# Performance work log

Measured on AMD Instinct MI355X. Metric: run time of the kernel, lower is better.

## Reference

```python
import jax, jax.numpy as jnp
import numpy as np
import math

B, N, D, H, CD = 2, 384, 256, 8, 3
HD = D // H

def _linear_init(key, out_f, in_f):
    k1, k2 = jax.random.split(key)
    bound = 1.0 / math.sqrt(in_f)
    w = jax.random.uniform(k1, (out_f, in_f), jnp.float32, -bound, bound)
    b = jax.random.uniform(k2, (out_f,), jnp.float32, -bound, bound)
    return w, b

def setup_inputs() -> dict:
    key = jax.random.key(0)
    ks = jax.random.split(key, 7)
    x = jax.random.normal(ks[0], (B, N, D), jnp.float32)
    coords = jax.random.normal(ks[1], (B, N, CD), jnp.float32)
    qkv_w, qkv_b = _linear_init(ks[2], 3 * D, D)
    rb_w1, rb_b1 = _linear_init(ks[3], D, CD)
    rb_w2, rb_b2 = _linear_init(ks[4], H, D)
    rv_w1, rv_b1 = _linear_init(ks[5], D, CD)
    rv_w2, rv_b2 = _linear_init(ks[6], D, D)
    return {"x": x, "coords": coords, "qkv_w": qkv_w, "qkv_b": qkv_b,
            "rb_w1": rb_w1, "rb_b1": rb_b1, "rb_w2": rb_w2, "rb_b2": rb_b2,
            "rv_w1": rv_w1, "rv_b1": rv_b1, "rv_w2": rv_w2, "rv_b2": rv_b2}

def reference(x, coords, qkv_w, qkv_b, rb_w1, rb_b1, rb_w2, rb_b2, rv_w1, rv_b1, rv_w2, rv_b2):
    # QKV projection -> (B, H, N, HD) each
    qkv = x @ qkv_w.T + qkv_b
    q, k, v = jnp.split(qkv, 3, axis=-1)
    to_heads = lambda t: t.reshape(B, N, H, HD).transpose(0, 2, 1, 3)
    qh, kh, vh = to_heads(q), to_heads(k), to_heads(v)

    # pairwise relative coordinates: (B, N, N, CD)
    rel = coords[:, :, None, :] - coords[:, None, :, :]

    # rel_bias MLP: (B, N, N, H) -> (B, H, N, N)
    rel_bias = jax.nn.silu(rel @ rb_w1.T + rb_b1) @ rb_w2.T + rb_b2
    rel_bias = rel_bias.transpose(0, 3, 1, 2)

    # rel_value MLP: (B, N, N, D) -> (B, H, N, N, HD)
    rel_value = jax.nn.silu(rel @ rv_w1.T + rv_b1) @ rv_w2.T + rv_b2
    rel_value = rel_value.reshape(B, N, N, H, HD).transpose(0, 3, 1, 2, 4)

    # attn_mask=None path: all-true boolean mask -> additive term is zero
    scores = jnp.einsum('bhid,bhjd->bhij', qh, kh) / math.sqrt(float(HD)) + rel_bias
    weights = jax.nn.softmax(scores, axis=-1)

    base = jnp.einsum('bhij,bhjd->bhid', weights, vh)
    rel_context = jnp.einsum('bhij,bhijd->bhid', weights, rel_value)
    context = base + rel_context  # (B, H, N, HD)
    return context.transpose(0, 2, 1, 3).reshape(B, N, D)
```

## Files before the change

### kernel.cpp

```cpp
#include <hip/hip_runtime.h>
#include <math.h>

#define BB 2
#define NN 384
#define DD 256
#define HH 8
#define RN (BB * NN)
#define INV_SQRT_HD 0.17677669529663687f
#define LOG2E 1.4426950408889634f
#define NLN2 -0.6931471805599453f
#define QSCALE (INV_SQRT_HD * LOG2E)

#define W2_ST 264
#define T_ST  264
#define EB_ST 392

typedef float f32x4 __attribute__((ext_vector_type(4)));
typedef __bf16 bf16x8 __attribute__((ext_vector_type(8)));
typedef __bf16 bf16x4 __attribute__((ext_vector_type(4)));

__device__ __forceinline__ f32x4 mfma16(bf16x8 a, bf16x8 b, f32x4 c) {
    return __builtin_amdgcn_mfma_f32_16x16x32_bf16(a, b, c, 0, 0, 0);
}

__device__ __forceinline__ float hidp(float d) {
    float e = __builtin_amdgcn_exp2f(d);
    return d * __builtin_amdgcn_rcpf(1.0f + e);
}
__device__ __forceinline__ bf16x8 hid8(bf16x8 av, float4 a0, float4 a1) {
    bf16x8 r;
    r[0] = (__bf16)hidp((float)av[0] - a0.x);
    r[1] = (__bf16)hidp((float)av[1] - a0.y);
    r[2] = (__bf16)hidp((float)av[2] - a0.z);
    r[3] = (__bf16)hidp((float)av[3] - a0.w);
    r[4] = (__bf16)hidp((float)av[4] - a1.x);
    r[5] = (__bf16)hidp((float)av[5] - a1.y);
    r[6] = (__bf16)hidp((float)av[6] - a1.z);
    r[7] = (__bf16)hidp((float)av[7] - a1.w);
    return r;
}
__device__ __forceinline__ bf16x8 hid8s(bf16x8 av, float a) {
    bf16x8 r;
#pragma unroll
    for (int q = 0; q < 8; ++q) r[q] = (__bf16)hidp((float)av[q] - a);
    return r;
}
__device__ __forceinline__ bf16x8 pack8(float4 a, float4 b) {
    bf16x8 r;
    r[0] = (__bf16)a.x; r[1] = (__bf16)a.y; r[2] = (__bf16)a.z; r[3] = (__bf16)a.w;
    r[4] = (__bf16)b.x; r[5] = (__bf16)b.y; r[6] = (__bf16)b.z; r[7] = (__bf16)b.w;
    return r;
}
__device__ __forceinline__ float selv(f32x4 v, int r) {
    return (r == 0) ? v[0] : (r == 1) ? v[1] : (r == 2) ? v[2] : v[3];
}

__global__ __launch_bounds__(256) void prep_kernel(
    const float* __restrict__ x, const float* __restrict__ coords,
    const float* __restrict__ qkv_w, const float* __restrict__ qkv_b,
    const float* __restrict__ rb_w1, const float* __restrict__ rv_w1,
    const float* __restrict__ rb_w2,
    float* __restrict__ qb, __bf16* __restrict__ kbbf, __bf16* __restrict__ vT,
    __bf16* __restrict__ Arb, __bf16* __restrict__ ArvT, __bf16* __restrict__ Arv,
    __bf16* __restrict__ w2neg)
{
    int bid = blockIdx.x, tid = threadIdx.x;
    if (bid >= 1344) {
        int idx = tid * 8;
        float4 wa = *(const float4*)(rb_w2 + idx);
        float4 wb = *(const float4*)(rb_w2 + idx + 4);
        float4 na = make_float4(-wa.x, -wa.y, -wa.z, -wa.w);
        float4 nb = make_float4(-wb.x, -wb.y, -wb.z, -wb.w);
        *(bf16x8*)(w2neg + idx) = pack8(na, nb);
        return;
    }
    if (bid >= 576) {
        int r = bid - 576, c = tid;
        float cx = coords[r * 3 + 0], cy = coords[r * 3 + 1], cz = coords[r * 3 + 2];
        float ab = (cx * rb_w1[c * 3] + cy * rb_w1[c * 3 + 1] + cz * rb_w1[c * 3 + 2]) * LOG2E;
        float av = (cx * rv_w1[c * 3] + cy * rv_w1[c * 3 + 1] + cz * rv_w1[c * 3 + 2]) * LOG2E;
        Arb[r * DD + c] = (__bf16)ab;
        ArvT[c * RN + r] = (__bf16)av;
        Arv[r * DD + c] = (__bf16)av;
        return;
    }
    int mt = bid % 48, nb = bid / 48;
    int w = tid >> 6, l = tid & 63, lr = l & 15, lg = l >> 4;
    int m0 = mt * 16, n0 = nb * 64 + w * 16;
    const float* xr = x + (size_t)(m0 + lr) * DD;
    const float* wr = qkv_w + (size_t)(n0 + lr) * DD;
    f32x4 acc = {0.f, 0.f, 0.f, 0.f};
#pragma unroll
    for (int ks = 0; ks < 8; ++ks) {
        int c0 = ks * 32 + lg * 8;
        float4 xa = *(const float4*)(xr + c0);
        float4 xb = *(const float4*)(xr + c0 + 4);
        float4 wa = *(const float4*)(wr + c0);
        float4 wb = *(const float4*)(wr + c0 + 4);
        acc = mfma16(pack8(xa, xb), pack8(wa, wb), acc);
    }
    int col = n0 + lr;
    float bo = qkv_b[col];
    int part = col >> 8, o = col & 255;
#pragma unroll
    for (int r = 0; r < 4; ++r) {
        int m = m0 + lg * 4 + r;
        float v = acc[r] + bo;
        if (part == 0) {
            qb[(size_t)m * DD + o] = v * QSCALE;
        } else if (part == 1) {
            kbbf[(size_t)m * DD + o] = (__bf16)v;
        } else {
            int b = (m >= NN) ? 1 : 0;
            int n = m - b * NN;
            vT[(size_t)b * DD * NN + (size_t)o * NN + n] = (__bf16)v;
        }
    }
}

__global__ __launch_bounds__(256, 4) void k2a_kernel(
    const float* __restrict__ rb_b1, const __bf16* __restrict__ w2neg,
    const float* __restrict__ rb_b2,
    const float* __restrict__ qb, const __bf16* __restrict__ kbbf,
    const __bf16* __restrict__ Arb,
    __bf16* __restrict__ eG, float* __restrict__ Zpart)
{
    __shared__ __align__(16) __bf16 qsbf[2][DD];
    __shared__ __align__(16) float Apr[2][DD];
    __shared__ __align__(16) __bf16 w2bf[HH * W2_ST];
    __shared__ float redsm[4][2][HH];

    int tid = threadIdx.x;
    int bid = blockIdx.x;
    int gp = bid >> 1, half = bid & 1;
    int gi0 = gp * 2;
    int b = (gp >= 192) ? 1 : 0;

    qsbf[0][tid] = (__bf16)qb[(size_t)gi0 * DD + tid];
    qsbf[1][tid] = (__bf16)qb[(size_t)(gi0 + 1) * DD + tid];
    float b1l = rb_b1[tid] * LOG2E;
    Apr[0][tid] = (float)Arb[(size_t)gi0 * DD + tid] + b1l;
    Apr[1][tid] = (float)Arb[(size_t)(gi0 + 1) * DD + tid] + b1l;
    {
        int idx = tid * 8;
        *(bf16x8*)&w2bf[(idx >> 8) * W2_ST + (idx & 255)] =
            *(const bf16x8*)(w2neg + idx);
    }
    __syncthreads();

    int l = tid & 63, wv = tid >> 6;
    int lr = l & 15, lg = l >> 4;
    float rb2l = rb_b2[lr & 7] * LOG2E;

    int jb0 = half * 192 + wv * 16;
    int jb1 = jb0 + 64, jb2 = jb0 + 128;
    const __bf16* arbB = Arb + (size_t)b * NN * DD;
    const __bf16* kbB  = kbbf + (size_t)b * NN * DD;
    const __bf16* ar0 = arbB + (size_t)(jb0 + lr) * DD;
    const __bf16* ar1 = arbB + (size_t)(jb1 + lr) * DD;
    const __bf16* ar2 = arbB + (size_t)(jb2 + lr) * DD;
    const __bf16* kr0 = kbB  + (size_t)(jb0 + lr) * DD;
    const __bf16* kr1 = kbB  + (size_t)(jb1 + lr) * DD;
    const __bf16* kr2 = kbB  + (size_t)(jb2 + lr) * DD;
    const __bf16* wfp = &w2bf[(lr & 7) * W2_ST];

    bf16x8 qf0_reg = *(const bf16x8*)&qsbf[0][(lr & 7) * 32 + lg * 8];
    bf16x8 qf1_reg = *(const bf16x8*)&qsbf[1][(lr & 7) * 32 + lg * 8];
    bf16x8 zero8;
#pragma unroll
    for (int e = 0; e < 8; ++e) zero8[e] = (__bf16)0.f;

    f32x4 zzz = {0.f, 0.f, 0.f, 0.f};
    f32x4 a00 = zzz, a01 = zzz, a02 = zzz;
    f32x4 a10 = zzz, a11 = zzz, a12 = zzz;
#pragma unroll
    for (int ks = 0; ks < 8; ++ks) {
        int c0 = ks * 32 + lg * 8;
        bf16x8 v0 = *(const bf16x8*)(ar0 + c0);
        bf16x8 v1 = *(const bf16x8*)(ar1 + c0);
        bf16x8 v2 = *(const bf16x8*)(ar2 + c0);
        bf16x8 k0 = *(const bf16x8*)(kr0 + c0);
        bf16x8 k1 = *(const bf16x8*)(kr1 + c0);
        bf16x8 k2 = *(const bf16x8*)(kr2 + c0);
        bf16x8 wf = *(const bf16x8*)(wfp + c0);
        float4 p00 = *(const float4*)&Apr[0][c0];
        float4 p01 = *(const float4*)&Apr[0][c0 + 4];
        float4 p10 = *(const float4*)&Apr[1][c0];
        float4 p11 = *(const float4*)&Apr[1][c0 + 4];
        bf16x8 q0 = (lr == ks) ? qf0_reg : zero8;
        bf16x8 q1 = (lr == ks) ? qf1_reg : zero8;
        a00 = mfma16(hid8(v0, p00, p01), wf, a00);
        a10 = mfma16(hid8(v0, p10, p11), wf, a10);
        a01 = mfma16(hid8(v1, p00, p01), wf, a01);
        a11 = mfma16(hid8(v1, p10, p11), wf, a11);
        a02 = mfma16(hid8(v2, p00, p01), wf, a02);
        a12 = mfma16(hid8(v2, p10, p11), wf, a12);
        a00 = mfma16(k0, q0, a00);
        a10 = mfma16(k0, q1, a10);
        a01 = mfma16(k1, q0, a01);
        a11 = mfma16(k1, q1, a11);
        a02 = mfma16(k2, q0, a02);
        a12 = mfma16(k2, q1, a12);
    }

    float z0 = 0.f, z1 = 0.f;
#define FINTILE(ACC, GI, JB, ZACC) { \
        float e0 = __builtin_amdgcn_exp2f(ACC[0] + rb2l); \
        float e1 = __builtin_amdgcn_exp2f(ACC[1] + rb2l); \
        float e2 = __builtin_amdgcn_exp2f(ACC[2] + rb2l); \
        float e3 = __builtin_amdgcn_exp2f(ACC[3] + rb2l); \
        if (lr < 8) { \
            bf16x4 ev; \
            ev[0] = (__bf16)e0; ev[1] = (__bf16)e1; \
            ev[2] = (__bf16)e2; ev[3] = (__bf16)e3; \
            *(bf16x4*)&eG[((size_t)(GI) * HH + lr) * NN + (JB) + lg * 4] = ev; \
        } \
        float zs = e0 + e1 + e2 + e3; \
        zs += __shfl_xor(zs, 16); \
        zs += __shfl_xor(zs, 32); \
        ZACC += zs; }
    FINTILE(a00, gi0,     jb0, z0)
    FINTILE(a01, gi0,     jb1, z0)
    FINTILE(a02, gi0,     jb2, z0)
    FINTILE(a10, gi0 + 1, jb0, z1)
    FINTILE(a11, gi0 + 1, jb1, z1)
    FINTILE(a12, gi0 + 1, jb2, z1)
#undef FINTILE
    if (lg == 0 && lr < 8) {
        redsm[wv][0][lr] = z0;
        redsm[wv][1][lr] = z1;
    }
    __syncthreads();
    if (tid < 16) {
        int g = tid >> 3, h = tid & 7;
        Zpart[((size_t)(gi0 + g) * 2 + half) * 8 + h] =
            redsm[0][g][h] + redsm[1][g][h] + redsm[2][g][h] + redsm[3][g][h];
    }
}

__global__ __launch_bounds__(256, 4) void k2b_kernel(
    const float* __restrict__ rv_b1, const float* __restrict__ rv_w2,
    const __bf16* __restrict__ vT, const __bf16* __restrict__ ArvT,
    const __bf16* __restrict__ Arv, const __bf16* __restrict__ eG,
    float* __restrict__ rcpart, float* __restrict__ basef)
{
    __shared__ __align__(16) float Apv[2][DD];
    __shared__ __align__(16) float Tl[2][HH * T_ST];
    __shared__ __align__(16) __bf16 els[16 * EB_ST];

    int tid = threadIdx.x;
    int bid = blockIdx.x;
    int gp = bid >> 1, ch = bid & 1;
    int gi0 = gp * 2;
    int b = (gp >= 192) ? 1 : 0;

    float b1l = rv_b1[tid] * LOG2E;
    Apv[0][tid] = (float)Arv[(size_t)gi0 * DD + tid] + b1l;
    Apv[1][tid] = (float)Arv[(size_t)(gi0 + 1) * DD + tid] + b1l;
    {
        int r = tid >> 4, cg = tid & 15;
        const __bf16* src = eG + (size_t)(gi0 * 8 + r) * NN;
#pragma unroll
        for (int s = 0; s < 3; ++s) {
            int col = s * 128 + cg * 8;
            *(bf16x8*)&els[r * EB_ST + col] = *(const bf16x8*)(src + col);
        }
    }
    __syncthreads();

    int l = tid & 63, wv = tid >> 6;
    int lr = l & 15, lg = l >> 4;

    int c0 = ch * 128 + wv * 16 + lr;
    int c1 = c0 + 64;
    float ap00 = Apv[0][c0], ap01 = Apv[0][c1];
    float ap10 = Apv[1][c0], ap11 = Apv[1][c1];
    const __bf16* vr0 = ArvT + (size_t)c0 * RN + b * NN;
    const __bf16* vr1 = ArvT + (size_t)c1 * RN + b * NN;
    const __bf16* tv0 = vT + (size_t)b * DD * NN + (size_t)c0 * NN;
    const __bf16* tv1 = vT + (size_t)b * DD * NN + (size_t)c1 * NN;

    f32x4 zzz = {0.f, 0.f, 0.f, 0.f};
    f32x4 T00 = zzz, T01 = zzz, T10 = zzz, T11 = zzz;
    f32x4 B0 = zzz, B1 = zzz;
#pragma unroll
    for (int ks = 0; ks < 12; ++ks) {
        int j0 = ks * 32 + lg * 8;
        bf16x8 ef  = *(const bf16x8*)&els[lr * EB_ST + j0];
        bf16x8 av0 = *(const bf16x8*)(vr0 + j0);
        bf16x8 av1 = *(const bf16x8*)(vr1 + j0);
        bf16x8 w0  = *(const bf16x8*)(tv0 + j0);
        bf16x8 w1  = *(const bf16x8*)(tv1 + j0);
        T00 = mfma16(ef, hid8s(av0, ap00), T00);
        T01 = mfma16(ef, hid8s(av1, ap01), T01);
        T10 = mfma16(ef, hid8s(av0, ap10), T10);
        T11 = mfma16(ef, hid8s(av1, ap11), T11);
        B0  = mfma16(ef, w0, B0);
        B1  = mfma16(ef, w1, B1);
    }

    if (lg < 2) {
#pragma unroll
        for (int r = 0; r < 4; ++r) {
            int h = lg * 4 + r;
            Tl[0][h * T_ST + c0] = T00[r] * NLN2;
            Tl[0][h * T_ST + c1] = T01[r] * NLN2;
        }
    } else {
#pragma unroll
        for (int r = 0; r < 4; ++r) {
            int h = (lg - 2) * 4 + r;
            Tl[1][h * T_ST + c0] = T10[r] * NLN2;
            Tl[1][h * T_ST + c1] = T11[r] * NLN2;
        }
    }
    {
        int h0 = c0 >> 5;
        if (lg == (h0 >> 2))     basef[(size_t)gi0 * DD + c0]       = selv(B0, h0 & 3);
        if (lg == 2 + (h0 >> 2)) basef[(size_t)(gi0 + 1) * DD + c0] = selv(B0, h0 & 3);
        int h1 = c1 >> 5;
        if (lg == (h1 >> 2))     basef[(size_t)gi0 * DD + c1]       = selv(B1, h1 & 3);
        if (lg == 2 + (h1 >> 2)) basef[(size_t)(gi0 + 1) * DD + c1] = selv(B1, h1 & 3);
    }
    __syncthreads();

    {
        int o = tid, h = o >> 5;
        const float4* w2p = (const float4*)(rv_w2 + (size_t)o * DD);
        const float* t0 = &Tl[0][h * T_ST];
        const float* t1 = &Tl[1][h * T_ST];
        float a0 = 0.f, a1 = 0.f;
#pragma unroll 4
        for (int cc = 0; cc < 32; ++cc) {
            int cidx = ch * 32 + cc;
            float4 wv4 = w2p[cidx];
            float4 u0 = *(const float4*)&t0[cidx * 4];
            float4 u1 = *(const float4*)&t1[cidx * 4];
            a0 += wv4.x * u0.x + wv4.y * u0.y + wv4.z * u0.z + wv4.w * u0.w;
            a1 += wv4.x * u1.x + wv4.y * u1.y + wv4.z * u1.z + wv4.w * u1.w;
        }
        rcpart[((size_t)ch * RN + gi0) * DD + o] = a0;
        rcpart[((size_t)ch * RN + gi0 + 1) * DD + o] = a1;
    }
}

__global__ __launch_bounds__(256) void k2c_kernel(
    const float* __restrict__ rcpart, const float* __restrict__ basef,
    const float* __restrict__ Zpart, const float* __restrict__ rv_b2,
    float* __restrict__ out)
{
    int gi = blockIdx.x, o = threadIdx.x, h = o >> 5;
    float z = Zpart[(size_t)gi * 16 + h] + Zpart[(size_t)gi * 16 + 8 + h];
    float rc = rcpart[(size_t)gi * DD + o] + rcpart[((size_t)RN + gi) * DD + o];
    out[(size_t)gi * DD + o] =
        (rc + basef[(size_t)gi * DD + o]) * __builtin_amdgcn_rcpf(z) + rv_b2[o];
}

extern "C" void kernel_launch(void* const* d_in, const int* in_sizes, int n_in,
                              void* d_out, int out_size, void* d_ws, size_t ws_size,
                              hipStream_t stream) {
    const float* x      = (const float*)d_in[0];
    const float* coords = (const float*)d_in[1];
    const float* qkv_w  = (const float*)d_in[2];
    const float* qkv_b  = (const float*)d_in[3];
    const float* rb_w1  = (const float*)d_in[4];
    const float* rb_b1  = (const float*)d_in[5];
    const float* rb_w2  = (const float*)d_in[6];
    const float* rb_b2  = (const float*)d_in[7];
    const float* rv_w1  = (const float*)d_in[8];
    const float* rv_b1  = (const float*)d_in[9];
    const float* rv_w2  = (const float*)d_in[10];
    const float* rv_b2  = (const float*)d_in[11];
    float* out = (float*)d_out;

    float* ws = (float*)d_ws;
    const int PER = RN * DD;
    float* qb = ws;
    __bf16* bfb  = (__bf16*)(ws + PER);
    __bf16* kbbf = bfb;
    __bf16* vTb  = bfb + PER;
    __bf16* Arb  = bfb + 2 * PER;
    __bf16* ArvT = bfb + 3 * PER;
    __bf16* Arv  = bfb + 4 * PER;
    __bf16* eG   = bfb + 5 * (size_t)PER;
    float* Zpart = (float*)(eG + (size_t)RN * HH * NN);
    float* basef = Zpart + (size_t)RN * 2 * HH;
    float* rcpart = basef + PER;
    __bf16* w2neg = (__bf16*)(rcpart + 2 * (size_t)PER);

    prep_kernel<<<1345, 256, 0, stream>>>(x, coords, qkv_w, qkv_b,
                                          rb_w1, rv_w1, rb_w2,
                                          qb, kbbf, vTb, Arb, ArvT, Arv, w2neg);
    k2a_kernel<<<RN, 256, 0, stream>>>(rb_b1, w2neg, rb_b2,
                                       qb, kbbf, Arb, eG, Zpart);
    k2b_kernel<<<RN, 256, 0, stream>>>(rv_b1, rv_w2,
                                       vTb, ArvT, Arv, eG, rcpart, basef);
    k2c_kernel<<<RN, 256, 0, stream>>>(rcpart, basef, Zpart, rv_b2, out);
}
```

Before: 75.81 us.

## Process four query rows per block in attention kernels to reuse key-side loads

```diff
diff --git a/kernel.cpp b/kernel.cpp
--- a/kernel.cpp
+++ b/kernel.cpp
@@ -12,8 +12,8 @@
 #define QSCALE (INV_SQRT_HD * LOG2E)
 
 #define W2_ST 264
-#define T_ST  264
 #define EB_ST 392
+#define TB_ST 264
 
 typedef float f32x4 __attribute__((ext_vector_type(4)));
 typedef __bf16 bf16x8 __attribute__((ext_vector_type(8)));
@@ -125,22 +125,23 @@
     const __bf16* __restrict__ Arb,
     __bf16* __restrict__ eG, float* __restrict__ Zpart)
 {
-    __shared__ __align__(16) __bf16 qsbf[2][DD];
-    __shared__ __align__(16) float Apr[2][DD];
+    __shared__ __align__(16) __bf16 qsbf[4][DD];
+    __shared__ __align__(16) float Apr[4][DD];
     __shared__ __align__(16) __bf16 w2bf[HH * W2_ST];
-    __shared__ float redsm[4][2][HH];
+    __shared__ float redsm[4][4][HH];
 
     int tid = threadIdx.x;
     int bid = blockIdx.x;
-    int gp = bid >> 1, half = bid & 1;
-    int gi0 = gp * 2;
-    int b = (gp >= 192) ? 1 : 0;
-
-    qsbf[0][tid] = (__bf16)qb[(size_t)gi0 * DD + tid];
-    qsbf[1][tid] = (__bf16)qb[(size_t)(gi0 + 1) * DD + tid];
+    int gq = bid >> 1, half = bid & 1;
+    int gi0 = gq * 4;
+    int b = (gq >= 96) ? 1 : 0;
+
     float b1l = rb_b1[tid] * LOG2E;
-    Apr[0][tid] = (float)Arb[(size_t)gi0 * DD + tid] + b1l;
-    Apr[1][tid] = (float)Arb[(size_t)(gi0 + 1) * DD + tid] + b1l;
+#pragma unroll
+    for (int g = 0; g < 4; ++g) {
+        qsbf[g][tid] = (__bf16)qb[(size_t)(gi0 + g) * DD + tid];
+        Apr[g][tid] = (float)Arb[(size_t)(gi0 + g) * DD + tid] + b1l;
+    }
     {
         int idx = tid * 8;
         *(bf16x8*)&w2bf[(idx >> 8) * W2_ST + (idx & 255)] =
@@ -153,26 +154,31 @@
     float rb2l = rb_b2[lr & 7] * LOG2E;
 
     int jb0 = half * 192 + wv * 16;
-    int jb1 = jb0 + 64, jb2 = jb0 + 128;
     const __bf16* arbB = Arb + (size_t)b * NN * DD;
     const __bf16* kbB  = kbbf + (size_t)b * NN * DD;
     const __bf16* ar0 = arbB + (size_t)(jb0 + lr) * DD;
-    const __bf16* ar1 = arbB + (size_t)(jb1 + lr) * DD;
-    const __bf16* ar2 = arbB + (size_t)(jb2 + lr) * DD;
-    const __bf16* kr0 = kbB  + (size_t)(jb0 + lr) * DD;
-    const __bf16* kr1 = kbB  + (size_t)(jb1 + lr) * DD;
-    const __bf16* kr2 = kbB  + (size_t)(jb2 + lr) * DD;
+    const __bf16* ar1 = ar0 + (size_t)64 * DD;
+    const __bf16* ar2 = ar0 + (size_t)128 * DD;
+    const __bf16* kr0 = kbB + (size_t)(jb0 + lr) * DD;
+    const __bf16* kr1 = kr0 + (size_t)64 * DD;
+    const __bf16* kr2 = kr0 + (size_t)128 * DD;
     const __bf16* wfp = &w2bf[(lr & 7) * W2_ST];
 
-    bf16x8 qf0_reg = *(const bf16x8*)&qsbf[0][(lr & 7) * 32 + lg * 8];
-    bf16x8 qf1_reg = *(const bf16x8*)&qsbf[1][(lr & 7) * 32 + lg * 8];
+    bf16x8 qfr[4];
+#pragma unroll
+    for (int g = 0; g < 4; ++g)
+        qfr[g] = *(const bf16x8*)&qsbf[g][(lr & 7) * 32 + lg * 8];
     bf16x8 zero8;
 #pragma unroll
     for (int e = 0; e < 8; ++e) zero8[e] = (__bf16)0.f;
 
-    f32x4 zzz = {0.f, 0.f, 0.f, 0.f};
-    f32x4 a00 = zzz, a01 = zzz, a02 = zzz;
-    f32x4 a10 = zzz, a11 = zzz, a12 = zzz;
+    f32x4 acc[4][3];
+#pragma unroll
+    for (int g = 0; g < 4; ++g)
+#pragma unroll
+        for (int t = 0; t < 3; ++t)
+            acc[g][t] = (f32x4){0.f, 0.f, 0.f, 0.f};
+
 #pragma unroll
     for (int ks = 0; ks < 8; ++ks) {
         int c0 = ks * 32 + lg * 8;
@@ -183,55 +189,44 @@
         bf16x8 k1 = *(const bf16x8*)(kr1 + c0);
         bf16x8 k2 = *(const bf16x8*)(kr2 + c0);
         bf16x8 wf = *(const bf16x8*)(wfp + c0);
-        float4 p00 = *(const float4*)&Apr[0][c0];
-        float4 p01 = *(const float4*)&Apr[0][c0 + 4];
-        float4 p10 = *(const float4*)&Apr[1][c0];
-        float4 p11 = *(const float4*)&Apr[1][c0 + 4];
-        bf16x8 q0 = (lr == ks) ? qf0_reg : zero8;
-        bf16x8 q1 = (lr == ks) ? qf1_reg : zero8;
-        a00 = mfma16(hid8(v0, p00, p01), wf, a00);
-        a10 = mfma16(hid8(v0, p10, p11), wf, a10);
-        a01 = mfma16(hid8(v1, p00, p01), wf, a01);
-        a11 = mfma16(hid8(v1, p10, p11), wf, a11);
-        a02 = mfma16(hid8(v2, p00, p01), wf, a02);
-        a12 = mfma16(hid8(v2, p10, p11), wf, a12);
-        a00 = mfma16(k0, q0, a00);
-        a10 = mfma16(k0, q1, a10);
-        a01 = mfma16(k1, q0, a01);
-        a11 = mfma16(k1, q1, a11);
-        a02 = mfma16(k2, q0, a02);
-        a12 = mfma16(k2, q1, a12);
-    }
-
-    float z0 = 0.f, z1 = 0.f;
-#define FINTILE(ACC, GI, JB, ZACC) { \
-        float e0 = __builtin_amdgcn_exp2f(ACC[0] + rb2l); \
-        float e1 = __builtin_amdgcn_exp2f(ACC[1] + rb2l); \
-        float e2 = __builtin_amdgcn_exp2f(ACC[2] + rb2l); \
-        float e3 = __builtin_amdgcn_exp2f(ACC[3] + rb2l); \
-        if (lr < 8) { \
-            bf16x4 ev; \
-            ev[0] = (__bf16)e0; ev[1] = (__bf16)e1; \
-            ev[2] = (__bf16)e2; ev[3] = (__bf16)e3; \
-            *(bf16x4*)&eG[((size_t)(GI) * HH + lr) * NN + (JB) + lg * 4] = ev; \
-        } \
-        float zs = e0 + e1 + e2 + e3; \
-        zs += __shfl_xor(zs, 16); \
-        zs += __shfl_xor(zs, 32); \
-        ZACC += zs; }
-    FINTILE(a00, gi0,     jb0, z0)
-    FINTILE(a01, gi0,     jb1, z0)
-    FINTILE(a02, gi0,     jb2, z0)
-    FINTILE(a10, gi0 + 1, jb0, z1)
-    FINTILE(a11, gi0 + 1, jb1, z1)
-    FINTILE(a12, gi0 + 1, jb2, z1)
-#undef FINTILE
-    if (lg == 0 && lr < 8) {
-        redsm[wv][0][lr] = z0;
-        redsm[wv][1][lr] = z1;
+#pragma unroll
+        for (int g = 0; g < 4; ++g) {
+            float4 pa = *(const float4*)&Apr[g][c0];
+            float4 pb = *(const float4*)&Apr[g][c0 + 4];
+            bf16x8 qf = (lr == ks) ? qfr[g] : zero8;
+            acc[g][0] = mfma16(hid8(v0, pa, pb), wf, acc[g][0]);
+            acc[g][1] = mfma16(hid8(v1, pa, pb), wf, acc[g][1]);
+            acc[g][2] = mfma16(hid8(v2, pa, pb), wf, acc[g][2]);
+            acc[g][0] = mfma16(k0, qf, acc[g][0]);
+            acc[g][1] = mfma16(k1, qf, acc[g][1]);
+            acc[g][2] = mfma16(k2, qf, acc[g][2]);
+        }
+    }
+
+#pragma unroll
+    for (int g = 0; g < 4; ++g) {
+        float z = 0.f;
+#pragma unroll
+        for (int t = 0; t < 3; ++t) {
+            float e0 = __builtin_amdgcn_exp2f(acc[g][t][0] + rb2l);
+            float e1 = __builtin_amdgcn_exp2f(acc[g][t][1] + rb2l);
+            float e2 = __builtin_amdgcn_exp2f(acc[g][t][2] + rb2l);
+            float e3 = __builtin_amdgcn_exp2f(acc[g][t][3] + rb2l);
+            if (lr < 8) {
+                bf16x4 ev;
+                ev[0] = (__bf16)e0; ev[1] = (__bf16)e1;
+                ev[2] = (__bf16)e2; ev[3] = (__bf16)e3;
+                *(bf16x4*)&eG[((size_t)(gi0 + g) * HH + lr) * NN + jb0 + t * 64 + lg * 4] = ev;
+            }
+            float zs = e0 + e1 + e2 + e3;
+            zs += __shfl_xor(zs, 16);
+            zs += __shfl_xor(zs, 32);
+            z += zs;
+        }
+        if (lg == 0 && lr < 8) redsm[wv][g][lr] = z;
     }
     __syncthreads();
-    if (tid < 16) {
+    if (tid < 32) {
         int g = tid >> 3, h = tid & 7;
         Zpart[((size_t)(gi0 + g) * 2 + half) * 8 + h] =
             redsm[0][g][h] + redsm[1][g][h] + redsm[2][g][h] + redsm[3][g][h];
@@ -244,26 +239,28 @@
     const __bf16* __restrict__ Arv, const __bf16* __restrict__ eG,
     float* __restrict__ rcpart, float* __restrict__ basef)
 {
-    __shared__ __align__(16) float Apv[2][DD];
-    __shared__ __align__(16) float Tl[2][HH * T_ST];
-    __shared__ __align__(16) __bf16 els[16 * EB_ST];
+    __shared__ __align__(16) float Apv[4][DD];
+    __shared__ __align__(16) __bf16 Tb[4][HH * TB_ST];
+    __shared__ __align__(16) __bf16 els[32 * EB_ST];
 
     int tid = threadIdx.x;
     int bid = blockIdx.x;
-    int gp = bid >> 1, ch = bid & 1;
-    int gi0 = gp * 2;
-    int b = (gp >= 192) ? 1 : 0;
+    int gq = bid >> 1, ch = bid & 1;
+    int gi0 = gq * 4;
+    int b = (gq >= 96) ? 1 : 0;
 
     float b1l = rv_b1[tid] * LOG2E;
-    Apv[0][tid] = (float)Arv[(size_t)gi0 * DD + tid] + b1l;
-    Apv[1][tid] = (float)Arv[(size_t)(gi0 + 1) * DD + tid] + b1l;
+#pragma unroll
+    for (int g = 0; g < 4; ++g)
+        Apv[g][tid] = (float)Arv[(size_t)(gi0 + g) * DD + tid] + b1l;
     {
-        int r = tid >> 4, cg = tid & 15;
-        const __bf16* src = eG + (size_t)(gi0 * 8 + r) * NN;
-#pragma unroll
-        for (int s = 0; s < 3; ++s) {
-            int col = s * 128 + cg * 8;
-            *(bf16x8*)&els[r * EB_ST + col] = *(const bf16x8*)(src + col);
+        const __bf16* src = eG + (size_t)(gi0 * 8) * NN;
+#pragma unroll
+        for (int s = 0; s < 6; ++s) {
+            int idx = tid + s * 256;
+            int r = idx / 48, cc = idx - r * 48;
+            *(bf16x8*)&els[r * EB_ST + cc * 8] =
+                *(const bf16x8*)(src + (size_t)r * NN + cc * 8);
         }
     }
     __syncthreads();
@@ -273,74 +270,100 @@
 
     int c0 = ch * 128 + wv * 16 + lr;
     int c1 = c0 + 64;
-    float ap00 = Apv[0][c0], ap01 = Apv[0][c1];
-    float ap10 = Apv[1][c0], ap11 = Apv[1][c1];
+    float ap[4][2];
+#pragma unroll
+    for (int g = 0; g < 4; ++g) {
+        ap[g][0] = Apv[g][c0];
+        ap[g][1] = Apv[g][c1];
+    }
     const __bf16* vr0 = ArvT + (size_t)c0 * RN + b * NN;
     const __bf16* vr1 = ArvT + (size_t)c1 * RN + b * NN;
     const __bf16* tv0 = vT + (size_t)b * DD * NN + (size_t)c0 * NN;
     const __bf16* tv1 = vT + (size_t)b * DD * NN + (size_t)c1 * NN;
 
-    f32x4 zzz = {0.f, 0.f, 0.f, 0.f};
-    f32x4 T00 = zzz, T01 = zzz, T10 = zzz, T11 = zzz;
-    f32x4 B0 = zzz, B1 = zzz;
+    f32x4 T[4][2], Bk[2][2];
+#pragma unroll
+    for (int g = 0; g < 4; ++g) {
+        T[g][0] = (f32x4){0.f, 0.f, 0.f, 0.f};
+        T[g][1] = (f32x4){0.f, 0.f, 0.f, 0.f};
+    }
+    Bk[0][0] = Bk[0][1] = Bk[1][0] = Bk[1][1] = (f32x4){0.f, 0.f, 0.f, 0.f};
+
 #pragma unroll
     for (int ks = 0; ks < 12; ++ks) {
         int j0 = ks * 32 + lg * 8;
-        bf16x8 ef  = *(const bf16x8*)&els[lr * EB_ST + j0];
+        bf16x8 ef0 = *(const bf16x8*)&els[lr * EB_ST + j0];
+        bf16x8 ef1 = *(const bf16x8*)&els[(16 + lr) * EB_ST + j0];
         bf16x8 av0 = *(const bf16x8*)(vr0 + j0);
         bf16x8 av1 = *(const bf16x8*)(vr1 + j0);
         bf16x8 w0  = *(const bf16x8*)(tv0 + j0);
         bf16x8 w1  = *(const bf16x8*)(tv1 + j0);
-        T00 = mfma16(ef, hid8s(av0, ap00), T00);
-        T01 = mfma16(ef, hid8s(av1, ap01), T01);
-        T10 = mfma16(ef, hid8s(av0, ap10), T10);
-        T11 = mfma16(ef, hid8s(av1, ap11), T11);
-        B0  = mfma16(ef, w0, B0);
-        B1  = mfma16(ef, w1, B1);
-    }
-
-    if (lg < 2) {
-#pragma unroll
-        for (int r = 0; r < 4; ++r) {
-            int h = lg * 4 + r;
-            Tl[0][h * T_ST + c0] = T00[r] * NLN2;
-            Tl[0][h * T_ST + c1] = T01[r] * NLN2;
-        }
-    } else {
-#pragma unroll
-        for (int r = 0; r < 4; ++r) {
-            int h = (lg - 2) * 4 + r;
-            Tl[1][h * T_ST + c0] = T10[r] * NLN2;
-            Tl[1][h * T_ST + c1] = T11[r] * NLN2;
-        }
-    }
-    {
-        int h0 = c0 >> 5;
-        if (lg == (h0 >> 2))     basef[(size_t)gi0 * DD + c0]       = selv(B0, h0 & 3);
-        if (lg == 2 + (h0 >> 2)) basef[(size_t)(gi0 + 1) * DD + c0] = selv(B0, h0 & 3);
-        int h1 = c1 >> 5;
-        if (lg == (h1 >> 2))     basef[(size_t)gi0 * DD + c1]       = selv(B1, h1 & 3);
-        if (lg == 2 + (h1 >> 2)) basef[(size_t)(gi0 + 1) * DD + c1] = selv(B1, h1 & 3);
+#pragma unroll
+        for (int g = 0; g < 4; ++g) {
+            bf16x8 e = (g < 2) ? ef0 : ef1;
+            T[g][0] = mfma16(e, hid8s(av0, ap[g][0]), T[g][0]);
+            T[g][1] = mfma16(e, hid8s(av1, ap[g][1]), T[g][1]);
+        }
+        Bk[0][0] = mfma16(ef0, w0, Bk[0][0]);
+        Bk[0][1] = mfma16(ef0, w1, Bk[0][1]);
+        Bk[1][0] = mfma16(ef1, w0, Bk[1][0]);
+        Bk[1][1] = mfma16(ef1, w1, Bk[1][1]);
+    }
+
+#pragma unroll
+    for (int g = 0; g < 4; ++g) {
+        if (!(g & 1)) {
+            if (lg < 2) {
+#pragma unroll
+                for (int r = 0; r < 4; ++r) {
+                    int h = lg * 4 + r;
+                    Tb[g][h * TB_ST + c0] = (__bf16)(T[g][0][r] * NLN2);
+                    Tb[g][h * TB_ST + c1] = (__bf16)(T[g][1][r] * NLN2);
+                }
+            }
+        } else {
+            if (lg >= 2) {
+#pragma unroll
+                for (int r = 0; r < 4; ++r) {
+                    int h = (lg - 2) * 4 + r;
+                    Tb[g][h * TB_ST + c0] = (__bf16)(T[g][0][r] * NLN2);
+                    Tb[g][h * TB_ST + c1] = (__bf16)(T[g][1][r] * NLN2);
+                }
+            }
+        }
+    }
+#pragma unroll
+    for (int cs = 0; cs < 2; ++cs) {
+        int c = cs ? c1 : c0;
+        int h = c >> 5;
+        if (lg == (h >> 2)) {
+            basef[(size_t)(gi0 + 0) * DD + c] = selv(Bk[0][cs], h & 3);
+            basef[(size_t)(gi0 + 2) * DD + c] = selv(Bk[1][cs], h & 3);
+        }
+        if (lg == 2 + (h >> 2)) {
+            basef[(size_t)(gi0 + 1) * DD + c] = selv(Bk[0][cs], h & 3);
+            basef[(size_t)(gi0 + 3) * DD + c] = selv(Bk[1][cs], h & 3);
+        }
     }
     __syncthreads();
 
     {
         int o = tid, h = o >> 5;
         const float4* w2p = (const float4*)(rv_w2 + (size_t)o * DD);
-        const float* t0 = &Tl[0][h * T_ST];
-        const float* t1 = &Tl[1][h * T_ST];
-        float a0 = 0.f, a1 = 0.f;
+#pragma unroll
+        for (int g = 0; g < 4; ++g) {
+            const __bf16* trow = &Tb[g][h * TB_ST];
+            float a = 0.f;
 #pragma unroll 4
-        for (int cc = 0; cc < 32; ++cc) {
-            int cidx = ch * 32 + cc;
-            float4 wv4 = w2p[cidx];
-            float4 u0 = *(const float4*)&t0[cidx * 4];
-            float4 u1 = *(const float4*)&t1[cidx * 4];
-            a0 += wv4.x * u0.x + wv4.y * u0.y + wv4.z * u0.z + wv4.w * u0.w;
-            a1 += wv4.x * u1.x + wv4.y * u1.y + wv4.z * u1.z + wv4.w * u1.w;
-        }
-        rcpart[((size_t)ch * RN + gi0) * DD + o] = a0;
-        rcpart[((size_t)ch * RN + gi0 + 1) * DD + o] = a1;
+            for (int cc = 0; cc < 32; ++cc) {
+                int cidx = ch * 32 + cc;
+                float4 w4 = w2p[cidx];
+                bf16x4 u = *(const bf16x4*)&trow[cidx * 4];
+                a += w4.x * (float)u[0] + w4.y * (float)u[1]
+                   + w4.z * (float)u[2] + w4.w * (float)u[3];
+            }
+            rcpart[((size_t)ch * RN + gi0 + g) * DD + o] = a;
+        }
     }
 }
 
@@ -391,9 +414,9 @@
     prep_kernel<<<1345, 256, 0, stream>>>(x, coords, qkv_w, qkv_b,
                                           rb_w1, rv_w1, rb_w2,
                                           qb, kbbf, vTb, Arb, ArvT, Arv, w2neg);
-    k2a_kernel<<<RN, 256, 0, stream>>>(rb_b1, w2neg, rb_b2,
-                                       qb, kbbf, Arb, eG, Zpart);
-    k2b_kernel<<<RN, 256, 0, stream>>>(rv_b1, rv_w2,
-                                       vTb, ArvT, Arv, eG, rcpart, basef);
+    k2a_kernel<<<384, 256, 0, stream>>>(rb_b1, w2neg, rb_b2,
+                                        qb, kbbf, Arb, eG, Zpart);
+    k2b_kernel<<<384, 256, 0, stream>>>(rv_b1, rv_w2,
+                                        vTb, ArvT, Arv, eG, rcpart, basef);
     k2c_kernel<<<RN, 256, 0, stream>>>(rcpart, basef, Zpart, rv_b2, out);
 }
```

Result: slower. 108.6 us (+43.2%).

## Retile k2b to four query rows by 64 channels, bf16 T staging

Applied to the files above, without the earlier changes.

```diff
diff --git a/kernel.cpp b/kernel.cpp
--- a/kernel.cpp
+++ b/kernel.cpp
@@ -12,8 +12,8 @@
 #define QSCALE (INV_SQRT_HD * LOG2E)
 
 #define W2_ST 264
-#define T_ST  264
 #define EB_ST 392
+#define TB_ST 68
 
 typedef float f32x4 __attribute__((ext_vector_type(4)));
 typedef __bf16 bf16x8 __attribute__((ext_vector_type(8)));
@@ -244,103 +244,106 @@
     const __bf16* __restrict__ Arv, const __bf16* __restrict__ eG,
     float* __restrict__ rcpart, float* __restrict__ basef)
 {
-    __shared__ __align__(16) float Apv[2][DD];
-    __shared__ __align__(16) float Tl[2][HH * T_ST];
-    __shared__ __align__(16) __bf16 els[16 * EB_ST];
+    __shared__ __align__(16) __bf16 els[32 * EB_ST];
+    __shared__ __align__(16) __bf16 Tb[4][HH * TB_ST];
+    __shared__ float aps[4][64];
 
     int tid = threadIdx.x;
     int bid = blockIdx.x;
-    int gp = bid >> 1, ch = bid & 1;
-    int gi0 = gp * 2;
-    int b = (gp >= 192) ? 1 : 0;
-
-    float b1l = rv_b1[tid] * LOG2E;
-    Apv[0][tid] = (float)Arv[(size_t)gi0 * DD + tid] + b1l;
-    Apv[1][tid] = (float)Arv[(size_t)(gi0 + 1) * DD + tid] + b1l;
+    int gq = bid >> 2, cq = bid & 3;
+    int gi0 = gq * 4;
+    int b = (gq >= 96) ? 1 : 0;
+
     {
-        int r = tid >> 4, cg = tid & 15;
-        const __bf16* src = eG + (size_t)(gi0 * 8 + r) * NN;
-#pragma unroll
-        for (int s = 0; s < 3; ++s) {
-            int col = s * 128 + cg * 8;
-            *(bf16x8*)&els[r * EB_ST + col] = *(const bf16x8*)(src + col);
-        }
+        const __bf16* src = eG + (size_t)(gi0 * 8) * NN;
+#pragma unroll
+        for (int s = 0; s < 6; ++s) {
+            int idx = tid + s * 256;
+            int r = idx / 48, cc = idx - r * 48;
+            *(bf16x8*)&els[r * EB_ST + cc * 8] =
+                *(const bf16x8*)(src + (size_t)r * NN + cc * 8);
+        }
+    }
+    {
+        int g = tid >> 6, cl0 = tid & 63;
+        aps[g][cl0] = (float)Arv[(size_t)(gi0 + g) * DD + cq * 64 + cl0]
+                    + rv_b1[cq * 64 + cl0] * LOG2E;
     }
     __syncthreads();
 
     int l = tid & 63, wv = tid >> 6;
     int lr = l & 15, lg = l >> 4;
-
-    int c0 = ch * 128 + wv * 16 + lr;
-    int c1 = c0 + 64;
-    float ap00 = Apv[0][c0], ap01 = Apv[0][c1];
-    float ap10 = Apv[1][c0], ap11 = Apv[1][c1];
-    const __bf16* vr0 = ArvT + (size_t)c0 * RN + b * NN;
-    const __bf16* vr1 = ArvT + (size_t)c1 * RN + b * NN;
-    const __bf16* tv0 = vT + (size_t)b * DD * NN + (size_t)c0 * NN;
-    const __bf16* tv1 = vT + (size_t)b * DD * NN + (size_t)c1 * NN;
-
-    f32x4 zzz = {0.f, 0.f, 0.f, 0.f};
-    f32x4 T00 = zzz, T01 = zzz, T10 = zzz, T11 = zzz;
-    f32x4 B0 = zzz, B1 = zzz;
+    int cl = wv * 16 + lr;
+    int cglob = cq * 64 + cl;
+
+    float ap0 = aps[0][cl], ap1 = aps[1][cl], ap2 = aps[2][cl], ap3 = aps[3][cl];
+    const __bf16* vr = ArvT + (size_t)cglob * RN + b * NN;
+    const __bf16* tv = vT + (size_t)b * DD * NN + (size_t)cglob * NN;
+    const __bf16* e0p = &els[lr * EB_ST];
+    const __bf16* e1p = &els[(16 + lr) * EB_ST];
+
+    f32x4 zz = {0.f, 0.f, 0.f, 0.f};
+    f32x4 T0 = zz, T1 = zz, T2 = zz, T3 = zz, Bk0 = zz, Bk1 = zz;
 #pragma unroll
     for (int ks = 0; ks < 12; ++ks) {
         int j0 = ks * 32 + lg * 8;
-        bf16x8 ef  = *(const bf16x8*)&els[lr * EB_ST + j0];
-        bf16x8 av0 = *(const bf16x8*)(vr0 + j0);
-        bf16x8 av1 = *(const bf16x8*)(vr1 + j0);
-        bf16x8 w0  = *(const bf16x8*)(tv0 + j0);
-        bf16x8 w1  = *(const bf16x8*)(tv1 + j0);
-        T00 = mfma16(ef, hid8s(av0, ap00), T00);
-        T01 = mfma16(ef, hid8s(av1, ap01), T01);
-        T10 = mfma16(ef, hid8s(av0, ap10), T10);
-        T11 = mfma16(ef, hid8s(av1, ap11), T11);
-        B0  = mfma16(ef, w0, B0);
-        B1  = mfma16(ef, w1, B1);
+        bf16x8 ef0 = *(const bf16x8*)(e0p + j0);
+        bf16x8 ef1 = *(const bf16x8*)(e1p + j0);
+        bf16x8 av  = *(const bf16x8*)(vr + j0);
+        bf16x8 w   = *(const bf16x8*)(tv + j0);
+        T0 = mfma16(ef0, hid8s(av, ap0), T0);
+        T1 = mfma16(ef0, hid8s(av, ap1), T1);
+        T2 = mfma16(ef1, hid8s(av, ap2), T2);
+        T3 = mfma16(ef1, hid8s(av, ap3), T3);
+        Bk0 = mfma16(ef0, w, Bk0);
+        Bk1 = mfma16(ef1, w, Bk1);
     }
 
     if (lg < 2) {
 #pragma unroll
         for (int r = 0; r < 4; ++r) {
             int h = lg * 4 + r;
-            Tl[0][h * T_ST + c0] = T00[r] * NLN2;
-            Tl[0][h * T_ST + c1] = T01[r] * NLN2;
+            Tb[0][h * TB_ST + cl] = (__bf16)(T0[r] * NLN2);
+            Tb[2][h * TB_ST + cl] = (__bf16)(T2[r] * NLN2);
         }
     } else {
 #pragma unroll
         for (int r = 0; r < 4; ++r) {
             int h = (lg - 2) * 4 + r;
-            Tl[1][h * T_ST + c0] = T10[r] * NLN2;
-            Tl[1][h * T_ST + c1] = T11[r] * NLN2;
+            Tb[1][h * TB_ST + cl] = (__bf16)(T1[r] * NLN2);
+            Tb[3][h * TB_ST + cl] = (__bf16)(T3[r] * NLN2);
         }
     }
     {
-        int h0 = c0 >> 5;
-        if (lg == (h0 >> 2))     basef[(size_t)gi0 * DD + c0]       = selv(B0, h0 & 3);
-        if (lg == 2 + (h0 >> 2)) basef[(size_t)(gi0 + 1) * DD + c0] = selv(B0, h0 & 3);
-        int h1 = c1 >> 5;
-        if (lg == (h1 >> 2))     basef[(size_t)gi0 * DD + c1]       = selv(B1, h1 & 3);
-        if (lg == 2 + (h1 >> 2)) basef[(size_t)(gi0 + 1) * DD + c1] = selv(B1, h1 & 3);
+        int h0 = cglob >> 5;
+        int rr = h0 & 3;
+        if (lg == (h0 >> 2)) {
+            basef[(size_t)(gi0 + 0) * DD + cglob] = selv(Bk0, rr);
+            basef[(size_t)(gi0 + 2) * DD + cglob] = selv(Bk1, rr);
+        }
+        if (lg == 2 + (h0 >> 2)) {
+            basef[(size_t)(gi0 + 1) * DD + cglob] = selv(Bk0, rr);
+            basef[(size_t)(gi0 + 3) * DD + cglob] = selv(Bk1, rr);
+        }
     }
     __syncthreads();
 
     {
         int o = tid, h = o >> 5;
         const float4* w2p = (const float4*)(rv_w2 + (size_t)o * DD);
-        const float* t0 = &Tl[0][h * T_ST];
-        const float* t1 = &Tl[1][h * T_ST];
-        float a0 = 0.f, a1 = 0.f;
+#pragma unroll
+        for (int g = 0; g < 4; ++g) {
+            const __bf16* trow = &Tb[g][h * TB_ST];
+            float a = 0.f;
 #pragma unroll 4
-        for (int cc = 0; cc < 32; ++cc) {
-            int cidx = ch * 32 + cc;
-            float4 wv4 = w2p[cidx];
-            float4 u0 = *(const float4*)&t0[cidx * 4];
-            float4 u1 = *(const float4*)&t1[cidx * 4];
-            a0 += wv4.x * u0.x + wv4.y * u0.y + wv4.z * u0.z + wv4.w * u0.w;
-            a1 += wv4.x * u1.x + wv4.y * u1.y + wv4.z * u1.z + wv4.w * u1.w;
-        }
-        rcpart[((size_t)ch * RN + gi0) * DD + o] = a0;
-        rcpart[((size_t)ch * RN + gi0 + 1) * DD + o] = a1;
+            for (int cc2 = 0; cc2 < 16; ++cc2) {
+                float4 w4 = w2p[cq * 16 + cc2];
+                bf16x4 u = *(const bf16x4*)&trow[cc2 * 4];
+                a += w4.x * (float)u[0] + w4.y * (float)u[1]
+                   + w4.z * (float)u[2] + w4.w * (float)u[3];
+            }
+            rcpart[((size_t)cq * RN + gi0 + g) * DD + o] = a;
+        }
     }
 }
 
@@ -351,9 +354,10 @@
 {
     int gi = blockIdx.x, o = threadIdx.x, h = o >> 5;
     float z = Zpart[(size_t)gi * 16 + h] + Zpart[(size_t)gi * 16 + 8 + h];
-    float rc = rcpart[(size_t)gi * DD + o] + rcpart[((size_t)RN + gi) * DD + o];
-    out[(size_t)gi * DD + o] =
-        (rc + basef[(size_t)gi * DD + o]) * __builtin_amdgcn_rcpf(z) + rv_b2[o];
+    size_t io = (size_t)gi * DD + o;
+    const size_t SL = (size_t)RN * DD;
+    float rc = rcpart[io] + rcpart[SL + io] + rcpart[2 * SL + io] + rcpart[3 * SL + io];
+    out[io] = (rc + basef[io]) * __builtin_amdgcn_rcpf(z) + rv_b2[o];
 }
 
 extern "C" void kernel_launch(void* const* d_in, const int* in_sizes, int n_in,
@@ -386,7 +390,7 @@
     float* Zpart = (float*)(eG + (size_t)RN * HH * NN);
     float* basef = Zpart + (size_t)RN * 2 * HH;
     float* rcpart = basef + PER;
-    __bf16* w2neg = (__bf16*)(rcpart + 2 * (size_t)PER);
+    __bf16* w2neg = (__bf16*)(rcpart + 4 * (size_t)PER);
 
     prep_kernel<<<1345, 256, 0, stream>>>(x, coords, qkv_w, qkv_b,
                                           rb_w1, rv_w1, rb_w2,
```

Result: slower. 82.74 us (+9.2%).

## Store K, V and relative-coordinate operands in MFMA fragment-major layout

Applied to the files above, without the earlier changes.

```diff
diff --git a/kernel.cpp b/kernel.cpp
--- a/kernel.cpp
+++ b/kernel.cpp
@@ -21,6 +21,15 @@
 
 __device__ __forceinline__ f32x4 mfma16(bf16x8 a, bf16x8 b, f32x4 c) {
     return __builtin_amdgcn_mfma_f32_16x16x32_bf16(a, b, c, 0, 0, 0);
+}
+
+__device__ __forceinline__ size_t fA(int b, int j, int c) {
+    return ((((size_t)b * 24 + (j >> 4)) * 8 + (c >> 5)) * 64
+            + (((c & 31) >> 3) << 4) + (j & 15)) * 8 + (c & 7);
+}
+__device__ __forceinline__ size_t fB(int b, int c, int j) {
+    return ((((size_t)b * 16 + (c >> 4)) * 12 + (j >> 5)) * 64
+            + (((j & 31) >> 3) << 4) + (c & 15)) * 8 + (j & 7);
 }
 
 __device__ __forceinline__ float hidp(float d) {
@@ -60,8 +69,10 @@
     const float* __restrict__ qkv_w, const float* __restrict__ qkv_b,
     const float* __restrict__ rb_w1, const float* __restrict__ rv_w1,
     const float* __restrict__ rb_w2,
-    float* __restrict__ qb, __bf16* __restrict__ kbbf, __bf16* __restrict__ vT,
-    __bf16* __restrict__ Arb, __bf16* __restrict__ ArvT, __bf16* __restrict__ Arv,
+    float* __restrict__ qb,
+    __bf16* __restrict__ Arb, __bf16* __restrict__ Arv,
+    __bf16* __restrict__ Abf, __bf16* __restrict__ Kbf,
+    __bf16* __restrict__ Avf, __bf16* __restrict__ Vf,
     __bf16* __restrict__ w2neg)
 {
     int bid = blockIdx.x, tid = threadIdx.x;
@@ -76,12 +87,14 @@
     }
     if (bid >= 576) {
         int r = bid - 576, c = tid;
+        int bb = r / NN, jl = r - bb * NN;
         float cx = coords[r * 3 + 0], cy = coords[r * 3 + 1], cz = coords[r * 3 + 2];
         float ab = (cx * rb_w1[c * 3] + cy * rb_w1[c * 3 + 1] + cz * rb_w1[c * 3 + 2]) * LOG2E;
         float av = (cx * rv_w1[c * 3] + cy * rv_w1[c * 3 + 1] + cz * rv_w1[c * 3 + 2]) * LOG2E;
         Arb[r * DD + c] = (__bf16)ab;
-        ArvT[c * RN + r] = (__bf16)av;
         Arv[r * DD + c] = (__bf16)av;
+        Abf[fA(bb, jl, c)] = (__bf16)ab;
+        Avf[fB(bb, c, jl)] = (__bf16)av;
         return;
     }
     int mt = bid % 48, nb = bid / 48;
@@ -106,14 +119,14 @@
     for (int r = 0; r < 4; ++r) {
         int m = m0 + lg * 4 + r;
         float v = acc[r] + bo;
+        int bb = (m >= NN) ? 1 : 0;
+        int n = m - bb * NN;
         if (part == 0) {
             qb[(size_t)m * DD + o] = v * QSCALE;
         } else if (part == 1) {
-            kbbf[(size_t)m * DD + o] = (__bf16)v;
+            Kbf[fA(bb, n, o)] = (__bf16)v;
         } else {
-            int b = (m >= NN) ? 1 : 0;
-            int n = m - b * NN;
-            vT[(size_t)b * DD * NN + (size_t)o * NN + n] = (__bf16)v;
+            Vf[fB(bb, o, n)] = (__bf16)v;
         }
     }
 }
@@ -121,8 +134,8 @@
 __global__ __launch_bounds__(256, 4) void k2a_kernel(
     const float* __restrict__ rb_b1, const __bf16* __restrict__ w2neg,
     const float* __restrict__ rb_b2,
-    const float* __restrict__ qb, const __bf16* __restrict__ kbbf,
-    const __bf16* __restrict__ Arb,
+    const float* __restrict__ qb, const __bf16* __restrict__ Kbf,
+    const __bf16* __restrict__ Abf, const __bf16* __restrict__ Arb,
     __bf16* __restrict__ eG, float* __restrict__ Zpart)
 {
     __shared__ __align__(16) __bf16 qsbf[2][DD];
@@ -154,14 +167,13 @@
 
     int jb0 = half * 192 + wv * 16;
     int jb1 = jb0 + 64, jb2 = jb0 + 128;
-    const __bf16* arbB = Arb + (size_t)b * NN * DD;
-    const __bf16* kbB  = kbbf + (size_t)b * NN * DD;
-    const __bf16* ar0 = arbB + (size_t)(jb0 + lr) * DD;
-    const __bf16* ar1 = arbB + (size_t)(jb1 + lr) * DD;
-    const __bf16* ar2 = arbB + (size_t)(jb2 + lr) * DD;
-    const __bf16* kr0 = kbB  + (size_t)(jb0 + lr) * DD;
-    const __bf16* kr1 = kbB  + (size_t)(jb1 + lr) * DD;
-    const __bf16* kr2 = kbB  + (size_t)(jb2 + lr) * DD;
+    int jt0 = half * 12 + wv;
+    const __bf16* pA0 = Abf + ((size_t)(b * 24 + jt0) * 8) * 512 + (size_t)l * 8;
+    const __bf16* pA1 = pA0 + (size_t)4 * 4096;
+    const __bf16* pA2 = pA0 + (size_t)8 * 4096;
+    const __bf16* pK0 = Kbf + ((size_t)(b * 24 + jt0) * 8) * 512 + (size_t)l * 8;
+    const __bf16* pK1 = pK0 + (size_t)4 * 4096;
+    const __bf16* pK2 = pK0 + (size_t)8 * 4096;
     const __bf16* wfp = &w2bf[(lr & 7) * W2_ST];
 
     bf16x8 qf0_reg = *(const bf16x8*)&qsbf[0][(lr & 7) * 32 + lg * 8];
@@ -176,12 +188,13 @@
 #pragma unroll
     for (int ks = 0; ks < 8; ++ks) {
         int c0 = ks * 32 + lg * 8;
-        bf16x8 v0 = *(const bf16x8*)(ar0 + c0);
-        bf16x8 v1 = *(const bf16x8*)(ar1 + c0);
-        bf16x8 v2 = *(const bf16x8*)(ar2 + c0);
-        bf16x8 k0 = *(const bf16x8*)(kr0 + c0);
-        bf16x8 k1 = *(const bf16x8*)(kr1 + c0);
-        bf16x8 k2 = *(const bf16x8*)(kr2 + c0);
+        size_t fo = (size_t)ks * 512;
+        bf16x8 v0 = *(const bf16x8*)(pA0 + fo);
+        bf16x8 v1 = *(const bf16x8*)(pA1 + fo);
+        bf16x8 v2 = *(const bf16x8*)(pA2 + fo);
+        bf16x8 k0 = *(const bf16x8*)(pK0 + fo);
+        bf16x8 k1 = *(const bf16x8*)(pK1 + fo);
+        bf16x8 k2 = *(const bf16x8*)(pK2 + fo);
         bf16x8 wf = *(const bf16x8*)(wfp + c0);
         float4 p00 = *(const float4*)&Apr[0][c0];
         float4 p01 = *(const float4*)&Apr[0][c0 + 4];
@@ -240,7 +253,7 @@
 
 __global__ __launch_bounds__(256, 4) void k2b_kernel(
     const float* __restrict__ rv_b1, const float* __restrict__ rv_w2,
-    const __bf16* __restrict__ vT, const __bf16* __restrict__ ArvT,
+    const __bf16* __restrict__ Avf, const __bf16* __restrict__ Vf,
     const __bf16* __restrict__ Arv, const __bf16* __restrict__ eG,
     float* __restrict__ rcpart, float* __restrict__ basef)
 {
@@ -275,10 +288,11 @@
     int c1 = c0 + 64;
     float ap00 = Apv[0][c0], ap01 = Apv[0][c1];
     float ap10 = Apv[1][c0], ap11 = Apv[1][c1];
-    const __bf16* vr0 = ArvT + (size_t)c0 * RN + b * NN;
-    const __bf16* vr1 = ArvT + (size_t)c1 * RN + b * NN;
-    const __bf16* tv0 = vT + (size_t)b * DD * NN + (size_t)c0 * NN;
-    const __bf16* tv1 = vT + (size_t)b * DD * NN + (size_t)c1 * NN;
+    int t0 = ch * 8 + wv;
+    const __bf16* pAv0 = Avf + ((size_t)(b * 16 + t0) * 12) * 512 + (size_t)l * 8;
+    const __bf16* pAv1 = pAv0 + (size_t)4 * 6144;
+    const __bf16* pV0  = Vf + ((size_t)(b * 16 + t0) * 12) * 512 + (size_t)l * 8;
+    const __bf16* pV1  = pV0 + (size_t)4 * 6144;
 
     f32x4 zzz = {0.f, 0.f, 0.f, 0.f};
     f32x4 T00 = zzz, T01 = zzz, T10 = zzz, T11 = zzz;
@@ -286,11 +300,12 @@
 #pragma unroll
     for (int ks = 0; ks < 12; ++ks) {
         int j0 = ks * 32 + lg * 8;
+        size_t fo = (size_t)ks * 512;
         bf16x8 ef  = *(const bf16x8*)&els[lr * EB_ST + j0];
-        bf16x8 av0 = *(const bf16x8*)(vr0 + j0);
-        bf16x8 av1 = *(const bf16x8*)(vr1 + j0);
-        bf16x8 w0  = *(const bf16x8*)(tv0 + j0);
-        bf16x8 w1  = *(const bf16x8*)(tv1 + j0);
+        bf16x8 av0 = *(const bf16x8*)(pAv0 + fo);
+        bf16x8 av1 = *(const bf16x8*)(pAv1 + fo);
+        bf16x8 w0  = *(const bf16x8*)(pV0 + fo);
+        bf16x8 w1  = *(const bf16x8*)(pV1 + fo);
         T00 = mfma16(ef, hid8s(av0, ap00), T00);
         T01 = mfma16(ef, hid8s(av1, ap01), T01);
         T10 = mfma16(ef, hid8s(av0, ap10), T10);
@@ -327,15 +342,15 @@
     {
         int o = tid, h = o >> 5;
         const float4* w2p = (const float4*)(rv_w2 + (size_t)o * DD);
-        const float* t0 = &Tl[0][h * T_ST];
-        const float* t1 = &Tl[1][h * T_ST];
+        const float* t0p = &Tl[0][h * T_ST];
+        const float* t1p = &Tl[1][h * T_ST];
         float a0 = 0.f, a1 = 0.f;
 #pragma unroll 4
         for (int cc = 0; cc < 32; ++cc) {
             int cidx = ch * 32 + cc;
             float4 wv4 = w2p[cidx];
-            float4 u0 = *(const float4*)&t0[cidx * 4];
-            float4 u1 = *(const float4*)&t1[cidx * 4];
+            float4 u0 = *(const float4*)&t0p[cidx * 4];
+            float4 u1 = *(const float4*)&t1p[cidx * 4];
             a0 += wv4.x * u0.x + wv4.y * u0.y + wv4.z * u0.z + wv4.w * u0.w;
             a1 += wv4.x * u1.x + wv4.y * u1.y + wv4.z * u1.z + wv4.w * u1.w;
         }
@@ -377,12 +392,13 @@
     const int PER = RN * DD;
     float* qb = ws;
     __bf16* bfb  = (__bf16*)(ws + PER);
-    __bf16* kbbf = bfb;
-    __bf16* vTb  = bfb + PER;
-    __bf16* Arb  = bfb + 2 * PER;
-    __bf16* ArvT = bfb + 3 * PER;
-    __bf16* Arv  = bfb + 4 * PER;
-    __bf16* eG   = bfb + 5 * (size_t)PER;
+    __bf16* Arb  = bfb;
+    __bf16* Arv  = bfb + PER;
+    __bf16* Abf  = bfb + 2 * PER;
+    __bf16* Kbf  = bfb + 3 * PER;
+    __bf16* Avf  = bfb + 4 * PER;
+    __bf16* Vf   = bfb + 5 * (size_t)PER;
+    __bf16* eG   = bfb + 6 * (size_t)PER;
     float* Zpart = (float*)(eG + (size_t)RN * HH * NN);
     float* basef = Zpart + (size_t)RN * 2 * HH;
     float* rcpart = basef + PER;
@@ -390,10 +406,10 @@
 
     prep_kernel<<<1345, 256, 0, stream>>>(x, coords, qkv_w, qkv_b,
                                           rb_w1, rv_w1, rb_w2,
-                                          qb, kbbf, vTb, Arb, ArvT, Arv, w2neg);
+                                          qb, Arb, Arv, Abf, Kbf, Avf, Vf, w2neg);
     k2a_kernel<<<RN, 256, 0, stream>>>(rb_b1, w2neg, rb_b2,
-                                       qb, kbbf, Arb, eG, Zpart);
+                                       qb, Kbf, Abf, Arb, eG, Zpart);
     k2b_kernel<<<RN, 256, 0, stream>>>(rv_b1, rv_w2,
-                                       vTb, ArvT, Arv, eG, rcpart, basef);
+                                       Avf, Vf, Arv, eG, rcpart, basef);
     k2c_kernel<<<RN, 256, 0, stream>>>(rcpart, basef, Zpart, rv_b2, out);
 }
```

Result: faster. 71.60 us (median of 2 runs) (-5.5%).
